# Optimization experiments

Measured on AMD Instinct MI355X. Metric: run time of the kernel, lower is better.

Reference implementation:

```python
import jax, jax.numpy as jnp
import numpy as np

IN_FEATURES = 512
HIDDEN_DIM = 512
B, S = 8, 2048


def setup_inputs() -> dict:
    key = jax.random.key(0)
    ks = jax.random.split(key, 7)
    sc_in = 1.0 / np.sqrt(IN_FEATURES)
    return {
        "x": jax.random.normal(ks[0], (B, S, IN_FEATURES), dtype=jnp.float32),
        "Wq": jax.random.normal(ks[1], (IN_FEATURES, HIDDEN_DIM), dtype=jnp.float32) * sc_in,
        "bq": jax.random.normal(ks[2], (HIDDEN_DIM,), dtype=jnp.float32) * 0.01,
        "Wk": jax.random.normal(ks[3], (IN_FEATURES, HIDDEN_DIM), dtype=jnp.float32) * sc_in,
        "bk": jax.random.normal(ks[4], (HIDDEN_DIM,), dtype=jnp.float32) * 0.01,
        "Wv": jax.random.normal(ks[5], (IN_FEATURES, HIDDEN_DIM), dtype=jnp.float32) * sc_in,
        "bv": jax.random.normal(ks[6], (HIDDEN_DIM,), dtype=jnp.float32) * 0.01,
    }


def reference(x, Wq, bq, Wk, bk, Wv, bv):
    # x: [B, S, in_features]
    q = jnp.einsum("bsf,fh->bsh", x, Wq) + bq  # [B, S, H]
    k = jnp.einsum("bsf,fh->bsh", x, Wk) + bk
    v = jnp.einsum("bsf,fh->bsh", x, Wv) + bv
    scale = 1.0 / jnp.sqrt(jnp.asarray(q.shape[-1], dtype=q.dtype))
    scores = jnp.einsum("bqh,bkh->bqk", q, k) * scale  # [B, S, S]
    weights = jax.nn.softmax(scores, axis=-1)
    return jnp.einsum("bqk,bkh->bqh", weights, v)  # [B, S, H]
```

## Files before the change

kernel.cpp:

```cpp
#include <hip/hip_runtime.h>
#include <hip/hip_bf16.h>

typedef __bf16 bf16;
typedef __bf16 bf16x8 __attribute__((ext_vector_type(8)));
typedef float  f32x4  __attribute__((ext_vector_type(4)));

#define MFMA16(a,b,c) __builtin_amdgcn_mfma_f32_16x16x32_bf16((a),(b),(c),0,0,0)

static const int BATCH = 8;
static const int SEQ   = 2048;
static const int HID   = 512;
static const int MTOT  = BATCH * SEQ;

__device__ __forceinline__ void gl2lds16(const void* g, void* l) {
    __builtin_amdgcn_global_load_lds(
        (const __attribute__((address_space(1))) void*)g,
        (__attribute__((address_space(3))) void*)l, 16, 0, 0);
}

__global__ void k_convert_x(const float* __restrict__ x, bf16* __restrict__ xb, int n4) {
    int i = blockIdx.x * blockDim.x + threadIdx.x;
    int stride = gridDim.x * blockDim.x;
    for (; i < n4; i += stride) {
        float4 v = ((const float4*)x)[i];
        union { bf16 h[4]; uint2 u; } o;
        o.h[0] = (bf16)v.x; o.h[1] = (bf16)v.y; o.h[2] = (bf16)v.z; o.h[3] = (bf16)v.w;
        ((uint2*)xb)[i] = o.u;
    }
}

__global__ void k_transpose_w(const float* __restrict__ Wq, const float* __restrict__ Wk,
                              const float* __restrict__ Wv, bf16* __restrict__ wt) {
    int z = blockIdx.z;
    const float* W = (z == 0) ? Wq : (z == 1) ? Wk : Wv;
    bf16* WT = wt + (size_t)z * HID * HID;
    __shared__ float tile[32][33];
    int t  = threadIdx.x;
    int tx = t & 31, ty = t >> 5;
    int f0 = blockIdx.y * 32, h0 = blockIdx.x * 32;
    for (int i = 0; i < 32; i += 8)
        tile[ty + i][tx] = W[(size_t)(f0 + ty + i) * HID + h0 + tx];
    __syncthreads();
    for (int i = 0; i < 32; i += 8)
        WT[(size_t)(h0 + ty + i) * HID + f0 + tx] = (bf16)tile[tx][ty + i];
}

__global__ __launch_bounds__(256) void
k_qkv(const bf16* __restrict__ xb, const bf16* __restrict__ wt,
      const float* __restrict__ bq, const float* __restrict__ bk, const float* __restrict__ bv,
      bf16* __restrict__ qb, bf16* __restrict__ kb, bf16* __restrict__ vt) {
    __shared__ __align__(16) char sm[65536];
    int z = blockIdx.z;
    const bf16*  WT   = wt + (size_t)z * HID * HID;
    const float* bias = (z == 0) ? bq : (z == 1) ? bk : bv;
    float scale = (z == 0) ? 0.044194173824159216f : 1.0f;

    int m0 = blockIdx.y * 128, n0 = blockIdx.x * 128;
    int t = threadIdx.x;
    int w = t >> 6, lane = t & 63, quad = lane >> 4, l15 = lane & 15;
    int wr = w >> 1, wc = w & 1;

    int rowA = t >> 3;
    int chS  = (t & 7) ^ (rowA & 7);
    const char* xga = (const char*)xb + ((size_t)(m0 + rowA) * 512 + chS * 8) * 2;
    const char* wga = (const char*)WT + ((size_t)(n0 + rowA) * 512 + chS * 8) * 2;

    const char* aK0 = sm + (wr * 64 + l15) * 128 + ((quad ^ (l15 & 7)) * 16);
    const char* aK1 = sm + (wr * 64 + l15) * 128 + (((4 + quad) ^ (l15 & 7)) * 16);
    const char* bK0 = sm + 16384 + (wc * 64 + l15) * 128 + ((quad ^ (l15 & 7)) * 16);
    const char* bK1 = sm + 16384 + (wc * 64 + l15) * 128 + (((4 + quad) ^ (l15 & 7)) * 16);

    f32x4 acc[4][4] = {};

#define QSTAGE(S)                                                             \
    {                                                                         \
        _Pragma("unroll")                                                     \
        for (int i = 0; i < 4; i++)                                           \
            gl2lds16(xga + i * 32768, sm + (S) * 32768 + i * 4096 + w * 1024);\
        _Pragma("unroll")                                                     \
        for (int i = 0; i < 4; i++)                                           \
            gl2lds16(wga + i * 32768,                                         \
                     sm + (S) * 32768 + 16384 + i * 4096 + w * 1024);         \
        xga += 128; wga += 128;                                               \
    }

#define QCOMP(CUR)                                                            \
    {                                                                         \
        bf16x8 af[4], bfr[4];                                                 \
        _Pragma("unroll")                                                     \
        for (int mt = 0; mt < 4; mt++)                                        \
            af[mt] = *(const bf16x8*)(aK0 + mt * 2048 + (CUR) * 32768);       \
        _Pragma("unroll")                                                     \
        for (int nt = 0; nt < 4; nt++)                                        \
            bfr[nt] = *(const bf16x8*)(bK0 + nt * 2048 + (CUR) * 32768);      \
        _Pragma("unroll")                                                     \
        for (int mt = 0; mt < 4; mt++)                                        \
            _Pragma("unroll")                                                 \
            for (int nt = 0; nt < 4; nt++)                                    \
                acc[mt][nt] = MFMA16(af[mt], bfr[nt], acc[mt][nt]);           \
        _Pragma("unroll")                                                     \
        for (int mt = 0; mt < 4; mt++)                                        \
            af[mt] = *(const bf16x8*)(aK1 + mt * 2048 + (CUR) * 32768);       \
        _Pragma("unroll")                                                     \
        for (int nt = 0; nt < 4; nt++)                                        \
            bfr[nt] = *(const bf16x8*)(bK1 + nt * 2048 + (CUR) * 32768);      \
        _Pragma("unroll")                                                     \
        for (int mt = 0; mt < 4; mt++)                                        \
            _Pragma("unroll")                                                 \
            for (int nt = 0; nt < 4; nt++)                                    \
                acc[mt][nt] = MFMA16(af[mt], bfr[nt], acc[mt][nt]);           \
    }

    QSTAGE(0);
    __syncthreads();
    for (int ii = 0; ii < 4; ii++) {
        QSTAGE(1);
        QCOMP(0);
        __syncthreads();
        if (ii < 3) QSTAGE(0);
        QCOMP(1);
        __syncthreads();
    }
#undef QSTAGE
#undef QCOMP

    if (z < 2) {
        bf16* out = (z == 0) ? qb : kb;
#pragma unroll
        for (int nt = 0; nt < 4; nt++) {
            int col = n0 + wc * 64 + nt * 16 + l15;
            float bc = bias[col];
#pragma unroll
            for (int mt = 0; mt < 4; mt++) {
                int rowb = m0 + wr * 64 + mt * 16 + quad * 4;
#pragma unroll
                for (int r = 0; r < 4; r++) {
                    float v = (acc[mt][nt][r] + bc) * scale;
                    out[(size_t)(rowb + r) * HID + col] = (bf16)v;
                }
            }
        }
    } else {
        bf16* st = (bf16*)sm;
#pragma unroll
        for (int nt = 0; nt < 4; nt++) {
            int colL = wc * 64 + nt * 16 + l15;
            float bc = bias[n0 + colL];
#pragma unroll
            for (int mt = 0; mt < 4; mt++) {
                int rowL = wr * 64 + mt * 16 + quad * 4;
#pragma unroll
                for (int r = 0; r < 4; r++)
                    st[(size_t)colL * 136 + rowL + r] = (bf16)(acc[mt][nt][r] + bc);
            }
        }
        __syncthreads();
        int b  = m0 >> 11;
        int s0 = m0 & 2047;
        bf16* vbase = vt + ((size_t)b * HID + n0) * SEQ + s0;
#pragma unroll
        for (int i = 0; i < 8; i++) {
            int p = i * 256 + t;
            int colL = p >> 4, ch = p & 15;
            *(uint4*)((char*)vbase + (size_t)colL * SEQ * 2 + ch * 16) =
                *(const uint4*)&st[(size_t)colL * 136 + ch * 8];
        }
    }
}

__global__ __launch_bounds__(512, 2) void
k_attn(const bf16* __restrict__ qb, const bf16* __restrict__ kbuf,
       const bf16* __restrict__ vt, float* __restrict__ out) {
    __shared__ __align__(16) char smem[136832];
    char* sm = smem;

    int j = blockIdx.x;
    int b = j & 7, qblk = j >> 3;
    int t = threadIdx.x, w = t >> 6, lane = t & 63, quad = lane >> 4, l15 = lane & 15;
    int rg = w & 3, kg = w >> 2;

    const bf16* Qrow   = qb + ((size_t)b * SEQ + qblk * 64 + rg * 16) * HID;
    const bf16* Kbase  = kbuf + (size_t)b * SEQ * HID;
    const bf16* VTbase = vt + (size_t)b * HID * SEQ;

    const char* kE = sm + (kg * 16 + l15) * 1024 + ((quad ^ (l15 & 7)) * 16);
    const char* kO = sm + (kg * 16 + l15) * 1024 + (((4 + quad) ^ (l15 & 7)) * 16);
    char*       pW = sm + 131072 + (rg * 16 + quad * 4) * 80 + (kg * 16 + l15) * 2;
    const char* pR = sm + 131072 + l15 * 80 + quad * 16;
    const char* vA = sm + 65536 + w * 4096 + l15 * 64 + ((quad ^ (l15 & 3)) * 16);
    float*      mlx = (float*)(sm + 136192);

    const char* kgp = (const char*)Kbase + w * 1024 + ((lane ^ w) * 16);
    const char* vgp = (const char*)VTbase + (w * 16 + (lane >> 2)) * 4096
                      + (((lane & 3) ^ ((lane >> 2) & 3)) * 16);

    bf16x8 qf[16];
#pragma unroll
    for (int kt = 0; kt < 16; kt++)
        qf[kt] = *(const bf16x8*)&Qrow[(size_t)l15 * HID + kt * 32 + quad * 8];

    float l_acc[4] = {0.f, 0.f, 0.f, 0.f};
    f32x4 o_acc[16] = {};

    const int NIT = SEQ / 32;

#define STAGE(S)                                                              \
    {                                                                         \
        _Pragma("unroll")                                                     \
        for (int jj = 0; jj < 4; jj++)                                        \
            gl2lds16(kgp + jj * 8192,                                         \
                     sm + (S) * 32768 + jj * 8192 + w * 1024);                \
        _Pragma("unroll")                                                     \
        for (int jj = 0; jj < 4; jj++)                                        \
            gl2lds16(vgp + jj * 524288,                                       \
                     sm + 65536 + (S) * 32768 + jj * 8192 + w * 1024);        \
        kgp += 32768; vgp += 64;                                              \
    }

#define QKP(CUR)                                                              \
    {                                                                         \
        f32x4 sa = {}, sb = {};                                               \
        __builtin_amdgcn_s_setprio(1);                                        \
        _Pragma("unroll")                                                     \
        for (int kt = 0; kt < 16; kt += 2) {                                  \
            bf16x8 kfe = *(const bf16x8*)(kE + (kt >> 1) * 128 + (CUR) * 32768); \
            bf16x8 kfo = *(const bf16x8*)(kO + (kt >> 1) * 128 + (CUR) * 32768); \
            sa = MFMA16(qf[kt], kfe, sa);                                     \
            sb = MFMA16(qf[kt + 1], kfo, sb);                                 \
        }                                                                     \
        __builtin_amdgcn_s_setprio(0);                                        \
        _Pragma("unroll")                                                     \
        for (int r = 0; r < 4; r++) {                                         \
            float p = __expf(sa[r] + sb[r] - 8.0f);                           \
            l_acc[r] += p;                                                    \
            *(bf16*)(pW + r * 80) = (bf16)p;                                  \
        }                                                                     \
    }

#define PV(CUR)                                                               \
    {                                                                         \
        bf16x8 pa0 = *(const bf16x8*)(pR + 0 * 1280);                         \
        bf16x8 pa1 = *(const bf16x8*)(pR + 1 * 1280);                         \
        bf16x8 pa2 = *(const bf16x8*)(pR + 2 * 1280);                         \
        bf16x8 pa3 = *(const bf16x8*)(pR + 3 * 1280);                         \
        __builtin_amdgcn_s_setprio(1);                                        \
        _Pragma("unroll")                                                     \
        for (int hs = 0; hs < 4; hs++) {                                      \
            bf16x8 vf = *(const bf16x8*)(vA + hs * 1024 + (CUR) * 32768);     \
            o_acc[0 * 4 + hs] = MFMA16(pa0, vf, o_acc[0 * 4 + hs]);           \
            o_acc[1 * 4 + hs] = MFMA16(pa1, vf, o_acc[1 * 4 + hs]);           \
            o_acc[2 * 4 + hs] = MFMA16(pa2, vf, o_acc[2 * 4 + hs]);           \
            o_acc[3 * 4 + hs] = MFMA16(pa3, vf, o_acc[3 * 4 + hs]);           \
        }                                                                     \
        __builtin_amdgcn_s_setprio(0);                                        \
    }

#define BAR_A()                                                               \
    {                                                                         \
        asm volatile("s_waitcnt vmcnt(0)" ::: "memory");                      \
        __builtin_amdgcn_sched_barrier(0);                                    \
        __builtin_amdgcn_s_barrier();                                         \
        __builtin_amdgcn_sched_barrier(0);                                    \
    }

#define BAR_B()                                                               \
    {                                                                         \
        asm volatile("s_waitcnt lgkmcnt(0)" ::: "memory");                    \
        __builtin_amdgcn_sched_barrier(0);                                    \
        __builtin_amdgcn_s_barrier();                                         \
        __builtin_amdgcn_sched_barrier(0);                                    \
    }

    STAGE(0);

    for (int ii = 0; ii < NIT / 2; ii++) {
        BAR_A();
        STAGE(1);
        __builtin_amdgcn_sched_barrier(0);
        QKP(0);
        BAR_B();
        PV(0);
        BAR_A();
        if (ii < NIT / 2 - 1) STAGE(0);
        __builtin_amdgcn_sched_barrier(0);
        QKP(1);
        BAR_B();
        PV(1);
    }

    float lw[4];
#pragma unroll
    for (int r = 0; r < 4; r++) {
        float v = l_acc[r];
        for (int d = 1; d < 16; d <<= 1) v += __shfl_xor(v, d, 64);
        lw[r] = v;
    }
    __syncthreads();
    if (l15 == 0)
#pragma unroll
        for (int r = 0; r < 4; r++) mlx[kg * 64 + rg * 16 + quad * 4 + r] = lw[r];
    __syncthreads();

    float lt[4][4];
#pragma unroll
    for (int rgp = 0; rgp < 4; rgp++)
#pragma unroll
        for (int r = 0; r < 4; r++) {
            int row = rgp * 16 + quad * 4 + r;
            lt[rgp][r] = 1.0f / (mlx[row] + mlx[64 + row]);
        }
    float* obase = out + ((size_t)b * SEQ + qblk * 64) * HID + w * 64;
#pragma unroll
    for (int rgp = 0; rgp < 4; rgp++)
#pragma unroll
        for (int hs = 0; hs < 4; hs++)
#pragma unroll
            for (int r = 0; r < 4; r++)
                obase[(size_t)(rgp * 16 + quad * 4 + r) * HID + hs * 16 + l15] =
                    o_acc[rgp * 4 + hs][r] * lt[rgp][r];
#undef STAGE
#undef QKP
#undef PV
#undef BAR_A
#undef BAR_B
}

extern "C" void kernel_launch(void* const* d_in, const int* in_sizes, int n_in,
                              void* d_out, int out_size, void* d_ws, size_t ws_size,
                              hipStream_t stream) {
    const float* x  = (const float*)d_in[0];
    const float* Wq = (const float*)d_in[1];
    const float* bq = (const float*)d_in[2];
    const float* Wk = (const float*)d_in[3];
    const float* bk = (const float*)d_in[4];
    const float* Wv = (const float*)d_in[5];
    const float* bv = (const float*)d_in[6];
    float* out = (float*)d_out;

    char* ws = (char*)d_ws;
    const size_t SZ_XB = (size_t)MTOT * HID * 2;
    const size_t SZ_WT = (size_t)HID * HID * 2;
    bf16* xb = (bf16*)(ws);
    bf16* wt = (bf16*)(ws + SZ_XB);
    bf16* qb = (bf16*)(ws + SZ_XB + 3 * SZ_WT);
    bf16* kb = (bf16*)(ws + SZ_XB + 3 * SZ_WT + SZ_XB);
    bf16* vt = (bf16*)(ws + SZ_XB + 3 * SZ_WT + 2 * SZ_XB);

    k_convert_x<<<2048, 256, 0, stream>>>(x, xb, MTOT * HID / 4);
    k_transpose_w<<<dim3(16, 16, 3), 256, 0, stream>>>(Wq, Wk, Wv, wt);
    k_qkv<<<dim3(4, 128, 3), 256, 0, stream>>>(xb, wt, bq, bk, bv, qb, kb, vt);
    k_attn<<<256, 512, 0, stream>>>(qb, kb, vt, out);
}
```

Baseline: 235.6 us.

## Load V fragments directly to registers and double key tile per iteration

The attention loop now stages only K into LDS, using 64-key tiles (two sub-groups per wave), while V^T fragments are loaded from global memory straight into registers instead of going through LDS. The P buffer is widened to hold 64 keys per row and the PV step uses two k-slices per iteration, halving the number of loop iterations and barriers. This removes LDS traffic and capacity for V, which lets K tiles grow. The cost is more registers for V fragments and exposed global-load latency, since V loads are issued just before the barrier-separated compute. Higher register pressure may also reduce occupancy.

```diff
diff --git a/kernel.cpp b/kernel.cpp
--- a/kernel.cpp
+++ b/kernel.cpp
@@ -171,7 +171,7 @@
 __global__ __launch_bounds__(512, 2) void
 k_attn(const bf16* __restrict__ qb, const bf16* __restrict__ kbuf,
        const bf16* __restrict__ vt, float* __restrict__ out) {
-    __shared__ __align__(16) char smem[136832];
+    __shared__ __align__(16) char smem[142848];
     char* sm = smem;
 
     int j = blockIdx.x;
@@ -183,16 +183,15 @@
     const bf16* Kbase  = kbuf + (size_t)b * SEQ * HID;
     const bf16* VTbase = vt + (size_t)b * HID * SEQ;
 
-    const char* kE = sm + (kg * 16 + l15) * 1024 + ((quad ^ (l15 & 7)) * 16);
-    const char* kO = sm + (kg * 16 + l15) * 1024 + (((4 + quad) ^ (l15 & 7)) * 16);
-    char*       pW = sm + 131072 + (rg * 16 + quad * 4) * 80 + (kg * 16 + l15) * 2;
-    const char* pR = sm + 131072 + l15 * 80 + quad * 16;
-    const char* vA = sm + 65536 + w * 4096 + l15 * 64 + ((quad ^ (l15 & 3)) * 16);
-    float*      mlx = (float*)(sm + 136192);
+    const int PBASE = 131072;
+    const char* kEb = sm + (size_t)(kg * 32 + l15) * 1024 + ((quad ^ (l15 & 7)) * 16);
+    const char* kOb = sm + (size_t)(kg * 32 + l15) * 1024 + (((4 + quad) ^ (l15 & 7)) * 16);
+    char*       pWb = sm + PBASE + (rg * 16 + quad * 4) * 176 + kg * 64 + l15 * 2;
+    const char* pRb = sm + PBASE + l15 * 176 + quad * 16;
+    float*      mlx = (float*)(sm + 142336);
 
     const char* kgp = (const char*)Kbase + w * 1024 + ((lane ^ w) * 16);
-    const char* vgp = (const char*)VTbase + (w * 16 + (lane >> 2)) * 4096
-                      + (((lane & 3) ^ ((lane >> 2) & 3)) * 16);
+    const char* vgp = (const char*)VTbase + (size_t)(w * 64 + l15) * 4096 + quad * 16;
 
     bf16x8 qf[16];
 #pragma unroll
@@ -201,57 +200,71 @@
 
     float l_acc[4] = {0.f, 0.f, 0.f, 0.f};
     f32x4 o_acc[16] = {};
-
-    const int NIT = SEQ / 32;
+    bf16x8 vf[4][2];
+
+    const int NIT = SEQ / 64;
 
 #define STAGE(S)                                                              \
     {                                                                         \
         _Pragma("unroll")                                                     \
-        for (int jj = 0; jj < 4; jj++)                                        \
+        for (int jj = 0; jj < 8; jj++)                                        \
             gl2lds16(kgp + jj * 8192,                                         \
-                     sm + (S) * 32768 + jj * 8192 + w * 1024);                \
-        _Pragma("unroll")                                                     \
-        for (int jj = 0; jj < 4; jj++)                                        \
-            gl2lds16(vgp + jj * 524288,                                       \
-                     sm + 65536 + (S) * 32768 + jj * 8192 + w * 1024);        \
-        kgp += 32768; vgp += 64;                                              \
+                     sm + (S) * 65536 + jj * 8192 + w * 1024);                \
+        kgp += 65536;                                                         \
+    }
+
+#define VLOAD(TOFF)                                                           \
+    {                                                                         \
+        _Pragma("unroll")                                                     \
+        for (int hs = 0; hs < 4; hs++)                                        \
+            _Pragma("unroll")                                                 \
+            for (int ks = 0; ks < 2; ks++)                                    \
+                vf[hs][ks] = *(const bf16x8*)(vgp + hs * 65536 + ks * 64 + (TOFF)); \
     }
 
 #define QKP(CUR)                                                              \
     {                                                                         \
-        f32x4 sa = {}, sb = {};                                               \
+        _Pragma("unroll")                                                     \
+        for (int kgs = 0; kgs < 2; kgs++) {                                   \
+            f32x4 sa = {}, sb = {};                                           \
+            const char* ke = kEb + (CUR) * 65536 + kgs * 16384;               \
+            const char* ko = kOb + (CUR) * 65536 + kgs * 16384;               \
+            __builtin_amdgcn_s_setprio(1);                                    \
+            _Pragma("unroll")                                                 \
+            for (int kp = 0; kp < 8; kp++) {                                  \
+                bf16x8 kfe = *(const bf16x8*)(ke + kp * 128);                 \
+                bf16x8 kfo = *(const bf16x8*)(ko + kp * 128);                 \
+                sa = MFMA16(qf[2 * kp], kfe, sa);                             \
+                sb = MFMA16(qf[2 * kp + 1], kfo, sb);                         \
+            }                                                                 \
+            __builtin_amdgcn_s_setprio(0);                                    \
+            _Pragma("unroll")                                                 \
+            for (int r = 0; r < 4; r++) {                                     \
+                float p = __expf(sa[r] + sb[r] - 8.0f);                       \
+                l_acc[r] += p;                                                \
+                *(bf16*)(pWb + kgs * 32 + r * 176) = (bf16)p;                 \
+            }                                                                 \
+        }                                                                     \
+    }
+
+#define PV()                                                                  \
+    {                                                                         \
+        bf16x8 pa[4][2];                                                      \
+        _Pragma("unroll")                                                     \
+        for (int rgp = 0; rgp < 4; rgp++)                                     \
+            _Pragma("unroll")                                                 \
+            for (int ks = 0; ks < 2; ks++)                                    \
+                pa[rgp][ks] = *(const bf16x8*)(pRb + rgp * 2816 + ks * 64);   \
         __builtin_amdgcn_s_setprio(1);                                        \
         _Pragma("unroll")                                                     \
-        for (int kt = 0; kt < 16; kt += 2) {                                  \
-            bf16x8 kfe = *(const bf16x8*)(kE + (kt >> 1) * 128 + (CUR) * 32768); \
-            bf16x8 kfo = *(const bf16x8*)(kO + (kt >> 1) * 128 + (CUR) * 32768); \
-            sa = MFMA16(qf[kt], kfe, sa);                                     \
-            sb = MFMA16(qf[kt + 1], kfo, sb);                                 \
-        }                                                                     \
-        __builtin_amdgcn_s_setprio(0);                                        \
-        _Pragma("unroll")                                                     \
-        for (int r = 0; r < 4; r++) {                                         \
-            float p = __expf(sa[r] + sb[r] - 8.0f);                           \
-            l_acc[r] += p;                                                    \
-            *(bf16*)(pW + r * 80) = (bf16)p;                                  \
-        }                                                                     \
-    }
-
-#define PV(CUR)                                                               \
-    {                                                                         \
-        bf16x8 pa0 = *(const bf16x8*)(pR + 0 * 1280);                         \
-        bf16x8 pa1 = *(const bf16x8*)(pR + 1 * 1280);                         \
-        bf16x8 pa2 = *(const bf16x8*)(pR + 2 * 1280);                         \
-        bf16x8 pa3 = *(const bf16x8*)(pR + 3 * 1280);                         \
-        __builtin_amdgcn_s_setprio(1);                                        \
-        _Pragma("unroll")                                                     \
-        for (int hs = 0; hs < 4; hs++) {                                      \
-            bf16x8 vf = *(const bf16x8*)(vA + hs * 1024 + (CUR) * 32768);     \
-            o_acc[0 * 4 + hs] = MFMA16(pa0, vf, o_acc[0 * 4 + hs]);           \
-            o_acc[1 * 4 + hs] = MFMA16(pa1, vf, o_acc[1 * 4 + hs]);           \
-            o_acc[2 * 4 + hs] = MFMA16(pa2, vf, o_acc[2 * 4 + hs]);           \
-            o_acc[3 * 4 + hs] = MFMA16(pa3, vf, o_acc[3 * 4 + hs]);           \
-        }                                                                     \
+        for (int hs = 0; hs < 4; hs++)                                        \
+            _Pragma("unroll")                                                 \
+            for (int ks = 0; ks < 2; ks++) {                                  \
+                o_acc[0 * 4 + hs] = MFMA16(pa[0][ks], vf[hs][ks], o_acc[0 * 4 + hs]); \
+                o_acc[1 * 4 + hs] = MFMA16(pa[1][ks], vf[hs][ks], o_acc[1 * 4 + hs]); \
+                o_acc[2 * 4 + hs] = MFMA16(pa[2][ks], vf[hs][ks], o_acc[2 * 4 + hs]); \
+                o_acc[3 * 4 + hs] = MFMA16(pa[3][ks], vf[hs][ks], o_acc[3 * 4 + hs]); \
+            }                                                                 \
         __builtin_amdgcn_s_setprio(0);                                        \
     }
 
@@ -275,17 +288,22 @@
 
     for (int ii = 0; ii < NIT / 2; ii++) {
         BAR_A();
+        VLOAD(0);
+        __builtin_amdgcn_sched_barrier(0);
         STAGE(1);
         __builtin_amdgcn_sched_barrier(0);
         QKP(0);
         BAR_B();
-        PV(0);
+        PV();
         BAR_A();
+        VLOAD(128);
+        __builtin_amdgcn_sched_barrier(0);
         if (ii < NIT / 2 - 1) STAGE(0);
         __builtin_amdgcn_sched_barrier(0);
         QKP(1);
         BAR_B();
-        PV(1);
+        PV();
+        vgp += 256;
     }
 
     float lw[4];
@@ -319,6 +337,7 @@
                 obase[(size_t)(rgp * 16 + quad * 4 + r) * HID + hs * 16 + l15] =
                     o_acc[rgp * 4 + hs][r] * lt[rgp][r];
 #undef STAGE
+#undef VLOAD
 #undef QKP
 #undef PV
 #undef BAR_A
```

Result: slower. 256.8 us (+9.0%).
